# Kernel optimization log

Measured on AMD Instinct MI355X. Metric: run time of the kernel, lower is better.

Reference implementation:

```python
import jax, jax.numpy as jnp
from jax import lax
import numpy as np


def setup_inputs() -> dict:
    key = jax.random.key(0)
    k1, k2, k3, k4, k5 = jax.random.split(key, 5)
    bs, m, v, L, P = 2, 16, 16, 40320, 32
    preds = jax.random.normal(k1, (bs, m, v, L), dtype=jnp.float32)
    target = jax.random.normal(k2, (bs, v, L), dtype=jnp.float32)
    weights = jax.random.uniform(k3, (L,), dtype=jnp.float32)
    scale = jax.random.uniform(k4, (v,), dtype=jnp.float32)
    # binary-ish patch masks over grid points (float, as in the torch buffer)
    masks = (jax.random.uniform(k5, (P, L)) < 0.25).astype(jnp.float32)
    return {"preds": preds, "target": target, "weights": weights,
            "scale": scale, "masks": masks, "beta": 1}


def _energy_score(x, y, m, beta):
    # x: (bs, m, D) ensemble, y: (bs, D) observation
    diff = x - y[:, None, :]
    a = jnp.sqrt(jnp.sum(diff * diff, axis=-1))            # (bs, m)
    score_a = jnp.mean(jnp.sum(a ** beta, axis=-1)) / m
    # pairwise distances via Gram trick (cdist p=2)
    sq = jnp.sum(x * x, axis=-1)                            # (bs, m)
    g = jnp.einsum('bid,bjd->bij', x, x)                    # (bs, m, m)
    d2 = jnp.maximum(sq[:, :, None] + sq[:, None, :] - 2.0 * g, 0.0)
    pos = d2 > 0
    d = jnp.where(pos, jnp.sqrt(jnp.where(pos, d2, 1.0)), 0.0)
    score_b = jnp.mean(jnp.sum(d ** beta, axis=(1, 2))) / (2 * m * (m - 1))
    return score_a - score_b


def reference(preds, target, weights, scale, masks, beta):
    beta = float(beta)
    bs, m, v, L = preds.shape
    # buffer scaling as in forward()
    p = preds * scale[None, None, :, None] * weights        # (bs, m, v, L)
    t = target * scale[None, :, None] * weights             # (bs, v, L)

    def body(acc, mask):
        # rearrange 'bs m v latlon -> bs m (latlon v)'
        x = (p * mask).transpose(0, 1, 3, 2).reshape(bs, m, L * v)
        y = (t * mask).transpose(0, 2, 1).reshape(bs, L * v)
        return acc + _energy_score(x, y, m, beta), None

    total, _ = lax.scan(body, jnp.float32(0.0), masks)
    return total
```

## Files before the change

### kernel.cpp

```cpp
#include <hip/hip_runtime.h>
#include <math.h>

#define BS 2
#define M 16
#define V 16
#define NROWB 136
#define NROWS 272
#define PMASK 32
#define NPB 630
#define NE 8704
#define PBSTRIDE 8704
#define SPLIT 30
#define QPB 21

typedef __attribute__((ext_vector_type(8))) short bf16x8;
typedef __attribute__((ext_vector_type(4))) float f32x4;
typedef __attribute__((ext_vector_type(4))) unsigned int u32x4;

#define VMW(n) asm volatile("s_waitcnt vmcnt(" #n ")" ::: "memory")

static __device__ __forceinline__ unsigned short f2bf(float x) {
    unsigned int u = __float_as_uint(x);
    unsigned int r = (u + 0x7FFFu + ((u >> 16) & 1u)) >> 16;
    return (unsigned short)r;
}

static __device__ __forceinline__ void k1_stage(
    const float* __restrict__ preds, float* __restrict__ dst,
    int b, int v0, int l0, int L, int lane, int wave)
{
#pragma unroll
    for (int n = 0; n < 2; ++n) {
        int r0 = wave * 8 + n * 4;
        int r = r0 + (lane >> 4);
        int grow = b * 256 + (r >> 1) * 16 + v0 + (r & 1);
        const float* g = preds + (size_t)grow * L + l0 + (lane & 15) * 4;
        __builtin_amdgcn_global_load_lds(
            (const __attribute__((address_space(1))) unsigned int*)g,
            (__attribute__((address_space(3))) unsigned int*)(dst + r0 * 64),
            16, 0, 0);
    }
}

template<int W>
static __device__ __forceinline__ void k1_chunk(
    const float* __restrict__ xsb,
    const float* __restrict__ targ,
    const float* __restrict__ scl,
    float wl,
    int v0, int lane, float* __restrict__ acc)
{
    const int base = (W == 0) ? 0 : 34 * W - 16;
    const int npair = (W == 0) ? 18 : 34;
    const int aoff = (W == 0) ? 16 : 0;

#pragma unroll
    for (int vc = 0; vc < 2; ++vc) {
        const int v = v0 + vc;
        float s = scl[v] * wl;
        float x[M];
#pragma unroll
        for (int i = 0; i < M; ++i)
            x[i] = xsb[(i * 2 + vc) * 64 + lane] * s;
        if (W == 0) {
            float y = targ[v] * s;
#pragma unroll
            for (int i = 0; i < M; ++i) {
                float d = x[i] - y;
                acc[i] = fmaf(d, d, acc[i]);
            }
        }
        int k = 0;
#pragma unroll
        for (int i = 0; i < M; ++i) {
#pragma unroll
            for (int j = i + 1; j < M; ++j) {
                if (k >= base && k < base + npair) {
                    float d = x[i] - x[j];
                    acc[aoff + k - base] = fmaf(d, d, acc[aoff + k - base]);
                }
                ++k;
            }
        }
    }
}

__global__ __launch_bounds__(256, 2)
void k1_fused(const float* __restrict__ preds, const float* __restrict__ target,
              const float* __restrict__ weights, const float* __restrict__ scale,
              const float* __restrict__ masks, float* __restrict__ partial,
              float* __restrict__ out, int L)
{
    __shared__ float xs[8][2048];
    unsigned short* sld = (unsigned short*)&xs[0][0];

    const int t = (int)threadIdx.x;
    const int lane = t & 63, wave = t >> 6;
    const int pb = (int)blockIdx.x;
    const int b  = (int)blockIdx.y;
    const int l0 = pb * 64;

    if (pb == 0 && b == 0 && t == 0) out[0] = 0.0f;

    const size_t Ls = (size_t)L;

    const float wl = weights[l0 + lane];
    float scl[V];
#pragma unroll
    for (int v = 0; v < V; ++v) scl[v] = scale[v];
    float targ[V];
    if (wave == 0) {
#pragma unroll
        for (int v = 0; v < V; ++v)
            targ[v] = target[(size_t)(b * V + v) * Ls + l0 + lane];
    }
    VMW(0);
    __builtin_amdgcn_sched_barrier(0);

#pragma unroll
    for (int s = 0; s < 8; ++s)
        k1_stage(preds, &xs[s][0], b, s * 2, l0, L, lane, wave);
    __builtin_amdgcn_sched_barrier(0);

    float acc[34];
#pragma unroll
    for (int r = 0; r < 34; ++r) acc[r] = 0.0f;

#pragma unroll
    for (int s = 0; s < 8; ++s) {
        switch (s) {
            case 0: VMW(14); break;  case 1: VMW(12); break;
            case 2: VMW(10); break;  case 3: VMW(8);  break;
            case 4: VMW(6);  break;  case 5: VMW(4);  break;
            case 6: VMW(2);  break;  default: VMW(0); break;
        }
        __builtin_amdgcn_s_barrier();
        __builtin_amdgcn_sched_barrier(0);
        const float* xsb = &xs[s][0];
        switch (wave) {
            case 0: k1_chunk<0>(xsb, targ, scl, wl, s * 2, lane, acc); break;
            case 1: k1_chunk<1>(xsb, targ, scl, wl, s * 2, lane, acc); break;
            case 2: k1_chunk<2>(xsb, targ, scl, wl, s * 2, lane, acc); break;
            default: k1_chunk<3>(xsb, targ, scl, wl, s * 2, lane, acc); break;
        }
    }

    ((unsigned int*)sld)[136 * 32 + t] = 0;

#pragma unroll
    for (int r = 0; r < 34; ++r) {
        const int R = 34 * wave + r;
        sld[R * 64 + (lane ^ ((R & 7) << 3))] = f2bf(acc[r]);
    }
    __syncthreads();

    const int ntile = (wave == 3) ? 3 : 2;
    f32x4 pacc[3][2];
#pragma unroll
    for (int ti = 0; ti < 3; ++ti)
#pragma unroll
        for (int pt = 0; pt < 2; ++pt)
            pacc[ti][pt] = (f32x4){0.f, 0.f, 0.f, 0.f};

#pragma unroll
    for (int ks = 0; ks < 2; ++ks) {
        bf16x8 bfr[2];
#pragma unroll
        for (int pt = 0; pt < 2; ++pt) {
            const float* mp = masks + (size_t)(pt * 16 + (lane & 15)) * Ls
                            + l0 + ks * 32 + (lane >> 4) * 8;
            u32x4 m0 = *(const u32x4*)mp;
            u32x4 m1 = *(const u32x4*)(mp + 4);
            union { unsigned int u[4]; bf16x8 v; } bb;
            bb.u[0] = __builtin_amdgcn_perm(m0.y, m0.x, 0x07060302);
            bb.u[1] = __builtin_amdgcn_perm(m0.w, m0.z, 0x07060302);
            bb.u[2] = __builtin_amdgcn_perm(m1.y, m1.x, 0x07060302);
            bb.u[3] = __builtin_amdgcn_perm(m1.w, m1.z, 0x07060302);
            bfr[pt] = bb.v;
        }
#pragma unroll
        for (int ti = 0; ti < 3; ++ti) {
            if (ti >= ntile) continue;
            const int tile = (ti == 2) ? 8 : (wave + ti * 4);
            const bf16x8 a = *(const bf16x8*)&sld[
                (tile * 16 + (lane & 15)) * 64 +
                ((ks * 32 + (lane >> 4) * 8) ^ ((lane & 7) << 3))];
            pacc[ti][0] = __builtin_amdgcn_mfma_f32_16x16x32_bf16(
                a, bfr[0], pacc[ti][0], 0, 0, 0);
            pacc[ti][1] = __builtin_amdgcn_mfma_f32_16x16x32_bf16(
                a, bfr[1], pacc[ti][1], 0, 0, 0);
        }
    }

    float* P = partial + (size_t)(pb * 2 + b) * (NROWB * PMASK);
#pragma unroll
    for (int ti = 0; ti < 3; ++ti) {
        if (ti >= ntile) continue;
        const int tile = (ti == 2) ? 8 : (wave + ti * 4);
#pragma unroll
        for (int pt = 0; pt < 2; ++pt)
#pragma unroll
            for (int reg = 0; reg < 4; ++reg) {
                const int row = tile * 16 + (lane >> 4) * 4 + reg;
                if (row < NROWB)
                    P[row * 32 + pt * 16 + (lane & 15)] = pacc[ti][pt][reg];
            }
    }
}

__global__ __launch_bounds__(256, 2)
void k3a_reduce(const float* __restrict__ P, float* __restrict__ P2)
{
    const int t = (int)threadIdx.x;
    const int e = (int)blockIdx.x * 256 + t;
    const int spl = (int)blockIdx.y;

    const float* p = P + (size_t)(spl * QPB) * PBSTRIDE + e;
    float a0 = 0.f, a1 = 0.f, a2 = 0.f;
#pragma unroll
    for (int q = 0; q < QPB; q += 3) {
        a0 += p[(size_t)(q    ) * PBSTRIDE];
        a1 += p[(size_t)(q + 1) * PBSTRIDE];
        a2 += p[(size_t)(q + 2) * PBSTRIDE];
    }
    P2[(size_t)spl * NE + e] = (a0 + a1) + a2;
}

__global__ __launch_bounds__(256, 2)
void k3b_finalize(const float* __restrict__ P2, const int* __restrict__ beta_p,
                  float* __restrict__ out)
{
    const int t = (int)threadIdx.x;
    const int e = (int)blockIdx.x * 256 + t;

    float a0 = 0.f, a1 = 0.f, a2 = 0.f;
#pragma unroll
    for (int q = 0; q < SPLIT; q += 3) {
        a0 += P2[(size_t)(q    ) * NE + e];
        a1 += P2[(size_t)(q + 1) * NE + e];
        a2 += P2[(size_t)(q + 2) * NE + e];
    }
    float d2 = fmaxf((a0 + a1) + a2, 0.0f);
    float beta = (float)beta_p[0];
    float d = (beta == 1.0f) ? sqrtf(d2) : powf(d2, 0.5f * beta);

    const float wa = 1.0f / (float)(BS * M);
    const float wb = -1.0f / (float)(BS * M * (M - 1));
    const int row_g = e >> 5;
    const int local = row_g % NROWB;
    float sum = ((local < M) ? wa : wb) * d;

    const int lane = t & 63, wv = t >> 6;
#pragma unroll
    for (int off = 32; off > 0; off >>= 1)
        sum += __shfl_down(sum, off, 64);
    __shared__ float red[4];
    if (lane == 0) red[wv] = sum;
    __syncthreads();
    if (t == 0)
        atomicAdd(out, red[0] + red[1] + red[2] + red[3]);
}

extern "C" void kernel_launch(void* const* d_in, const int* in_sizes, int n_in,
                              void* d_out, int out_size, void* d_ws, size_t ws_size,
                              hipStream_t stream)
{
    const float* preds   = (const float*)d_in[0];
    const float* target  = (const float*)d_in[1];
    const float* weights = (const float*)d_in[2];
    const float* scale   = (const float*)d_in[3];
    const float* masks   = (const float*)d_in[4];
    const int*   beta    = (const int*)d_in[5];
    float* out = (float*)d_out;

    int L = in_sizes[2];

    float* partial = (float*)d_ws;
    size_t p_bytes = (size_t)NPB * 2 * NROWB * PMASK * sizeof(float);
    float* partial2 = (float*)((char*)d_ws + ((p_bytes + 255) & ~(size_t)255));

    dim3 g1(NPB, BS);
    k1_fused<<<g1, 256, 0, stream>>>(preds, target, weights, scale, masks,
                                     partial, out, L);

    dim3 g3a(NE / 256, SPLIT);
    k3a_reduce<<<g3a, 256, 0, stream>>>(partial, partial2);

    k3b_finalize<<<NE / 256, 256, 0, stream>>>(partial2, beta, out);
}
```

Baseline: 155.9 us.

## Replace direct-to-LDS staging with register-prefetched double-buffered LDS pipeline

Instead of issuing all eight stages as global_load_lds into a 64KB shared buffer up front, the kernel now prefetches three stages ahead into registers and writes them into a two-slot LDS ring, with one barrier per stage. This cuts LDS use from about 64KB to about 34KB, which could let more blocks share a CU and improve occupancy. In exchange it spends extra VGPRs on the prefetch buffers, adds explicit LDS writes, and loses the up-front issue of all loads, so the loads in flight per block are limited.

```diff
diff --git a/kernel.cpp b/kernel.cpp
--- a/kernel.cpp
+++ b/kernel.cpp
@@ -18,6 +18,7 @@
 typedef __attribute__((ext_vector_type(4))) unsigned int u32x4;
 
 #define VMW(n) asm volatile("s_waitcnt vmcnt(" #n ")" ::: "memory")
+#define LGKM0  asm volatile("s_waitcnt lgkmcnt(0)" ::: "memory")
 
 static __device__ __forceinline__ unsigned short f2bf(float x) {
     unsigned int u = __float_as_uint(x);
@@ -25,20 +26,26 @@
     return (unsigned short)r;
 }
 
-static __device__ __forceinline__ void k1_stage(
-    const float* __restrict__ preds, float* __restrict__ dst,
+static __device__ __forceinline__ void k1_issue(
+    const float* __restrict__ preds, f32x4* __restrict__ r,
     int b, int v0, int l0, int L, int lane, int wave)
 {
 #pragma unroll
     for (int n = 0; n < 2; ++n) {
         int r0 = wave * 8 + n * 4;
-        int r = r0 + (lane >> 4);
-        int grow = b * 256 + (r >> 1) * 16 + v0 + (r & 1);
-        const float* g = preds + (size_t)grow * L + l0 + (lane & 15) * 4;
-        __builtin_amdgcn_global_load_lds(
-            (const __attribute__((address_space(1))) unsigned int*)g,
-            (__attribute__((address_space(3))) unsigned int*)(dst + r0 * 64),
-            16, 0, 0);
+        int rr = r0 + (lane >> 4);
+        int grow = b * 256 + (rr >> 1) * 16 + v0 + (rr & 1);
+        r[n] = *(const f32x4*)(preds + (size_t)grow * L + l0 + (lane & 15) * 4);
+    }
+}
+
+static __device__ __forceinline__ void k1_write(
+    float* __restrict__ dst, const f32x4* __restrict__ r, int lane, int wave)
+{
+#pragma unroll
+    for (int n = 0; n < 2; ++n) {
+        int r0 = wave * 8 + n * 4;
+        *(f32x4*)(dst + r0 * 64 + lane * 4) = r[n];
     }
 }
 
@@ -91,8 +98,8 @@
               const float* __restrict__ masks, float* __restrict__ partial,
               float* __restrict__ out, int L)
 {
-    __shared__ float xs[8][2048];
-    unsigned short* sld = (unsigned short*)&xs[0][0];
+    __shared__ float xs[2][2048];
+    __shared__ unsigned short sld[144 * 64];
 
     const int t = (int)threadIdx.x;
     const int lane = t & 63, wave = t >> 6;
@@ -117,10 +124,16 @@
     VMW(0);
     __builtin_amdgcn_sched_barrier(0);
 
-#pragma unroll
-    for (int s = 0; s < 8; ++s)
-        k1_stage(preds, &xs[s][0], b, s * 2, l0, L, lane, wave);
+    f32x4 rb[3][2];
+    k1_issue(preds, rb[0], b, 0, l0, L, lane, wave);
+    k1_issue(preds, rb[1], b, 2, l0, L, lane, wave);
+    k1_issue(preds, rb[2], b, 4, l0, L, lane, wave);
     __builtin_amdgcn_sched_barrier(0);
+    VMW(4);
+    k1_write(&xs[0][0], rb[0], lane, wave);
+    LGKM0;
+    __builtin_amdgcn_s_barrier();
+    __builtin_amdgcn_sched_barrier(0);
 
     float acc[34];
 #pragma unroll
@@ -128,21 +141,26 @@
 
 #pragma unroll
     for (int s = 0; s < 8; ++s) {
-        switch (s) {
-            case 0: VMW(14); break;  case 1: VMW(12); break;
-            case 2: VMW(10); break;  case 3: VMW(8);  break;
-            case 4: VMW(6);  break;  case 5: VMW(4);  break;
-            case 6: VMW(2);  break;  default: VMW(0); break;
-        }
-        __builtin_amdgcn_s_barrier();
-        __builtin_amdgcn_sched_barrier(0);
-        const float* xsb = &xs[s][0];
+        if (s + 3 < 8) {
+            k1_issue(preds, rb[(s + 3) % 3], b, (s + 3) * 2, l0, L, lane, wave);
+            __builtin_amdgcn_sched_barrier(0);
+        }
+        const float* xsb = &xs[s & 1][0];
         switch (wave) {
             case 0: k1_chunk<0>(xsb, targ, scl, wl, s * 2, lane, acc); break;
             case 1: k1_chunk<1>(xsb, targ, scl, wl, s * 2, lane, acc); break;
             case 2: k1_chunk<2>(xsb, targ, scl, wl, s * 2, lane, acc); break;
             default: k1_chunk<3>(xsb, targ, scl, wl, s * 2, lane, acc); break;
         }
+        if (s + 1 < 8) {
+            if (s < 5)       { VMW(4); }
+            else if (s == 5) { VMW(2); }
+            else             { VMW(0); }
+            k1_write(&xs[(s + 1) & 1][0], rb[(s + 1) % 3], lane, wave);
+        }
+        LGKM0;
+        __builtin_amdgcn_s_barrier();
+        __builtin_amdgcn_sched_barrier(0);
     }
 
     ((unsigned int*)sld)[136 * 32 + t] = 0;
```

New measurement: 153.6 us. About the same (-1.5%).
